# Optimization experiments

Hardware: AMD Instinct MI355X
Metric: run time of the kernel (lower is better)

The kernel has to match this reference:

```python
import jax, jax.numpy as jnp
import numpy as np

EMB = 1024
HEADS = 16
HEAD_DIM = EMB // HEADS


def setup_inputs() -> dict:
    key = jax.random.key(0)
    ks = jax.random.split(key, 12)
    B, S = 4, 2048
    s = 1.0 / np.sqrt(EMB)
    inp = {
        "query": jax.random.normal(ks[0], (B, S, EMB), jnp.float32),
        "key": jax.random.normal(ks[1], (B, S, EMB), jnp.float32),
        "value": jax.random.normal(ks[2], (B, S, EMB), jnp.float32),
        "mask": jax.random.randint(ks[3], (B, 1, 1, S), 0, 2) > 0,
        "Wq": jax.random.normal(ks[4], (EMB, EMB), jnp.float32) * s,
        "bq": jax.random.normal(ks[5], (EMB,), jnp.float32) * s,
        "Wk": jax.random.normal(ks[6], (EMB, EMB), jnp.float32) * s,
        "bk": jax.random.normal(ks[7], (EMB,), jnp.float32) * s,
        "Wv": jax.random.normal(ks[8], (EMB, EMB), jnp.float32) * s,
        "bv": jax.random.normal(ks[9], (EMB,), jnp.float32) * s,
        "Wo": jax.random.normal(ks[10], (EMB, EMB), jnp.float32) * s,
        "bo": jax.random.normal(ks[11], (EMB,), jnp.float32) * s,
    }
    return inp


def _split(x):
    # (B, S, E) -> (B, H, S, D)
    B, S, _ = x.shape
    return x.reshape(B, S, HEADS, HEAD_DIM).transpose(0, 2, 1, 3)


def reference(query, key, value, mask, Wq, bq, Wk, bk, Wv, bv, Wo, bo):
    q = _split(query @ Wq + bq)
    k = _split(key @ Wk + bk)
    v = _split(value @ Wv + bv)
    scale = 1.0 / np.sqrt(HEAD_DIM).astype(np.float32)
    # (B, H, S, S) score matrix, explicitly materialized as in the original
    scores = jnp.einsum("bhqd,bhkd->bhqk", q, k) * scale
    scores = jnp.where(mask, scores, -jnp.inf)
    probs = jax.nn.softmax(scores, axis=-1)
    attn = jnp.einsum("bhqk,bhkd->bhqd", probs, v)
    B, _, S, _ = attn.shape
    out = attn.transpose(0, 2, 1, 3).reshape(B, S, EMB)
    return out @ Wo + bo
```

## Files before the change

kernel.cpp:

```cpp
#include <hip/hip_runtime.h>
#include <hip/hip_bf16.h>
#include <stdint.h>

#define EMB 1024
#define HEADS 16
#define HDIM 64
#define BATCH 4
#define SEQ 2048
#define MTOT (BATCH * SEQ)

typedef unsigned short u16;
typedef __attribute__((ext_vector_type(8))) short bf16x8;
typedef __attribute__((ext_vector_type(4))) float f32x4;

__device__ inline u16 f2bf(float f) {
    uint32_t u = __builtin_bit_cast(uint32_t, f);
    u += 0x7fffu + ((u >> 16) & 1u);
    return (u16)(u >> 16);
}

__device__ inline uint32_t pk2bf(float a, float b) {
    uint32_t ua = __builtin_bit_cast(uint32_t, a) + 0x8000u;
    uint32_t ub = __builtin_bit_cast(uint32_t, b) + 0x8000u;
    return (ua >> 16) | (ub & 0xffff0000u);
}

__device__ inline f32x4 mfma16(bf16x8 a, bf16x8 b, f32x4 c) {
    return __builtin_amdgcn_mfma_f32_16x16x32_bf16(a, b, c, 0, 0, 0);
}

#define GLDS16(gp, lp)                                                        \
    __builtin_amdgcn_global_load_lds(                                         \
        (const __attribute__((address_space(1))) void*)(gp),                  \
        (__attribute__((address_space(3))) void*)(lp), 16, 0, 0)

__global__ void mask_compact(const int* __restrict__ mask,
                             int* __restrict__ cnt, int* __restrict__ idx,
                             float* __restrict__ Msg) {
    __shared__ int ps[256];
    const int b = blockIdx.x, tid = threadIdx.x;
    const int* mp = mask + (size_t)b * SEQ;
    int m[8], s = 0;
#pragma unroll
    for (int e = 0; e < 8; ++e) {
        m[e] = mp[tid * 8 + e] ? 1 : 0;
        s += m[e];
    }
    ps[tid] = s;
    __syncthreads();
    for (int off = 1; off < 256; off <<= 1) {
        int v = (tid >= off) ? ps[tid - off] : 0;
        __syncthreads();
        if (tid >= off) ps[tid] += v;
        __syncthreads();
    }
    const int total = ps[255];
    int r = ps[tid] - s;
#pragma unroll
    for (int e = 0; e < 8; ++e)
        if (m[e]) idx[b * SEQ + r++] = tid * 8 + e;
    if (tid == 0) cnt[b] = total;
    for (int j = tid; j < SEQ; j += 256)
        Msg[b * SEQ + j] = (j < total) ? 0.0f : -30000.0f;
}

__global__ void gather_cast(const float* __restrict__ src,
                            const int* __restrict__ idx,
                            const int* __restrict__ cnt,
                            u16* __restrict__ dst) {
    const int row = blockIdx.x;
    const int b = row >> 11, j = row & (SEQ - 1);
    const int cn = cnt[b];
    const int cp = (cn + 127) & ~127;
    if (j >= cp) return;
    const int c4 = threadIdx.x;
    float4 v = {0.f, 0.f, 0.f, 0.f};
    if (j < cn) {
        const int srow = idx[b * SEQ + j];
        v = ((const float4*)(src + (size_t)(b * SEQ + srow) * EMB))[c4];
    }
    ushort4 o;
    o.x = f2bf(v.x); o.y = f2bf(v.y); o.z = f2bf(v.z); o.w = f2bf(v.w);
    ((ushort4*)(dst + (size_t)row * EMB))[c4] = o;
}

__global__ void cast_f32_bf16(const float* __restrict__ src,
                              u16* __restrict__ dst, int n4) {
    int i = blockIdx.x * blockDim.x + threadIdx.x;
    if (i >= n4) return;
    float4 v = ((const float4*)src)[i];
    ushort4 o;
    o.x = f2bf(v.x); o.y = f2bf(v.y); o.z = f2bf(v.z); o.w = f2bf(v.w);
    ((ushort4*)dst)[i] = o;
}

__global__ void transpose_cast(const float* __restrict__ W,
                               u16* __restrict__ Wt) {
    __shared__ u16 T[64][65];
    const int kb = blockIdx.y * 64, nb = blockIdx.x * 64;
    const int tr = threadIdx.x >> 4;
    const int tc = (threadIdx.x & 15) * 4;
#pragma unroll
    for (int j = 0; j < 4; ++j) {
        int r = tr + j * 16;
        float4 v = *(const float4*)&W[(size_t)(kb + r) * EMB + nb + tc];
        T[tc + 0][r] = f2bf(v.x);
        T[tc + 1][r] = f2bf(v.y);
        T[tc + 2][r] = f2bf(v.z);
        T[tc + 3][r] = f2bf(v.w);
    }
    __syncthreads();
#pragma unroll
    for (int j = 0; j < 4; ++j) {
        int rr = tr + j * 16;
        ushort4 o;
        o.x = T[rr][tc]; o.y = T[rr][tc + 1];
        o.z = T[rr][tc + 2]; o.w = T[rr][tc + 3];
        *(ushort4*)&Wt[(size_t)(nb + rr) * EMB + kb + tc] = o;
    }
}

__global__ void transpose_v(const u16* __restrict__ Vp, u16* __restrict__ Vt,
                            const int* __restrict__ cnt) {
    __shared__ u16 T[64][65];
    const int h = blockIdx.x;
    const int b = blockIdx.y >> 5;
    const int s0 = (blockIdx.y & 31) * 64;
    const int cp = (cnt[b] + 127) & ~127;
    if (s0 >= cp) return;
    const int tr = threadIdx.x >> 3;
    const int tc = (threadIdx.x & 7) * 8;
#pragma unroll
    for (int j = 0; j < 2; ++j) {
        int sr = tr + j * 32;
        uint4 v = *(const uint4*)&Vp[(size_t)(b * SEQ + s0 + sr) * EMB +
                                     h * 64 + tc];
        const u16* p = (const u16*)&v;
#pragma unroll
        for (int e = 0; e < 8; ++e) T[tc + e][sr] = p[e];
    }
    __syncthreads();
#pragma unroll
    for (int j = 0; j < 2; ++j) {
        int d = tr + j * 32;
        u16 tmp[8];
#pragma unroll
        for (int e = 0; e < 8; ++e) tmp[e] = T[d][tc + e];
        const int base32 = s0 + (tc & 32);
        const int p0 = ((tc & 8) << 1) + ((tc & 16) >> 2);
        const size_t rowoff =
            ((size_t)(b * HEADS + h) * HDIM + d) * SEQ;
        *(uint2*)&Vt[rowoff + base32 + p0] = *(const uint2*)&tmp[0];
        *(uint2*)&Vt[rowoff + base32 + p0 + 8] = *(const uint2*)&tmp[4];
    }
}

template <bool OUT_BF16>
__global__ __launch_bounds__(256, 2) void gemm_bt(
    const u16* __restrict__ A, const u16* __restrict__ Bt,
    const float* __restrict__ bias, void* __restrict__ C,
    int M, int N, int K, const int* __restrict__ cnt) {
    __shared__ __align__(16) u16 As[128 * 32];
    __shared__ __align__(16) u16 Bs[128 * 32];
    const int m0 = blockIdx.y * 128, n0 = blockIdx.x * 128;
    if (cnt) {
        const int bb = m0 >> 11;
        const int cp = (cnt[bb] + 127) & ~127;
        if ((m0 & (SEQ - 1)) >= cp) return;
    }
    const int tid = threadIdx.x;
    const int w = tid >> 6, l = tid & 63;
    const int quad = l >> 4, l16 = l & 15;
    const int wm = (w >> 1) * 64, wn = (w & 1) * 64;

    f32x4 acc[4][4];
#pragma unroll
    for (int i = 0; i < 4; ++i)
#pragma unroll
        for (int j = 0; j < 4; ++j) acc[i][j] = (f32x4){0.f, 0.f, 0.f, 0.f};

    for (int k0 = 0; k0 < K; k0 += 32) {
        __syncthreads();
#pragma unroll
        for (int i = 0; i < 2; ++i) {
            int c = (w * 2 + i) * 64 + l;
            int r = c >> 2;
            int sc = (c & 3) ^ ((r >> 1) & 3);
            GLDS16(A + (size_t)(m0 + r) * K + k0 + sc * 8, &As[c * 8]);
            GLDS16(Bt + (size_t)(n0 + r) * K + k0 + sc * 8, &Bs[c * 8]);
        }
        __syncthreads();
        bf16x8 af[4], bfr[4];
#pragma unroll
        for (int mt = 0; mt < 4; ++mt) {
            int ra = wm + mt * 16 + l16;
            af[mt] = *(const bf16x8*)&As[ra * 32 +
                                         ((quad ^ ((ra >> 1) & 3)) * 8)];
        }
#pragma unroll
        for (int nt = 0; nt < 4; ++nt) {
            int rb = wn + nt * 16 + l16;
            bfr[nt] = *(const bf16x8*)&Bs[rb * 32 +
                                          ((quad ^ ((rb >> 1) & 3)) * 8)];
        }
#pragma unroll
        for (int mt = 0; mt < 4; ++mt)
#pragma unroll
            for (int nt = 0; nt < 4; ++nt)
                acc[mt][nt] = mfma16(af[mt], bfr[nt], acc[mt][nt]);
    }

#pragma unroll
    for (int mt = 0; mt < 4; ++mt) {
#pragma unroll
        for (int nt = 0; nt < 4; ++nt) {
            int col = n0 + wn + nt * 16 + l16;
            float bv = bias[col];
#pragma unroll
            for (int r = 0; r < 4; ++r) {
                int row = m0 + wm + mt * 16 + quad * 4 + r;
                float v = acc[mt][nt][r] + bv;
                if (OUT_BF16)
                    ((u16*)C)[(size_t)row * N + col] = f2bf(v);
                else
                    ((float*)C)[(size_t)row * N + col] = v;
            }
        }
    }
}

__global__ __launch_bounds__(256, 2) void attn_kernel(
    const u16* __restrict__ Qp, const u16* __restrict__ Kp,
    const u16* __restrict__ Vt, const float* __restrict__ Msg,
    const int* __restrict__ cnt, u16* __restrict__ attnb) {
    __shared__ __align__(16) u16 Ks[2][128 * 64];
    __shared__ __align__(16) u16 Vts[2][64 * 128];
    __shared__ __align__(16) float Ms[SEQ];

    const int tid = threadIdx.x;
    const int w = tid >> 6, l = tid & 63;
    const int quad = l >> 4, l16 = l & 15;

    const int nqb = SEQ / 128;
    const int qb = blockIdx.x % nqb;
    const int bh = blockIdx.x / nqb;
    const int b = bh / HEADS, h = bh % HEADS;
    const int q0 = qb * 128;
    const size_t head_off = (size_t)b * SEQ * EMB + (size_t)h * HDIM;
    const size_t vt_off = (size_t)bh * HDIM * SEQ;

    const int ntile = ((cnt[b] + 127) & ~127) >> 7;

    auto stageKV = [&](int buf, int t) {
#pragma unroll
        for (int i = 0; i < 4; ++i) {
            int c = (w * 4 + i) * 64 + l;
            int r = c >> 3;
            int sc = (c & 7) ^ (r & 7);
            GLDS16(Kp + head_off + (size_t)(t * 128 + r) * EMB + sc * 8,
                   &Ks[buf][c * 8]);
        }
#pragma unroll
        for (int i = 0; i < 4; ++i) {
            int c = (w * 4 + i) * 64 + l;
            int r = c >> 4;
            int sc = (c & 15) ^ (r & 15);
            GLDS16(Vt + vt_off + (size_t)r * SEQ + t * 128 + sc * 8,
                   &Vts[buf][c * 8]);
        }
    };

    bf16x8 bq[2][2];
#pragma unroll
    for (int g = 0; g < 2; ++g) {
        const u16* qrow =
            Qp + head_off + (size_t)(q0 + w * 32 + g * 16 + l16) * EMB;
        bq[g][0] = *(const bf16x8*)(qrow + quad * 8);
        bq[g][1] = *(const bf16x8*)(qrow + 32 + quad * 8);
    }

    {
        const float4* mg = (const float4*)(Msg + (size_t)b * SEQ);
        const int nf4 = ntile * 32;
        for (int j = tid; j < nf4; j += 256) ((float4*)Ms)[j] = mg[j];
    }
    stageKV(0, 0);
    __syncthreads();

    f32x4 OA[4], OB[4];
#pragma unroll
    for (int i = 0; i < 4; ++i) {
        OA[i] = (f32x4){0.f, 0.f, 0.f, 0.f};
        OB[i] = (f32x4){0.f, 0.f, 0.f, 0.f};
    }
    float lA = 0.f, lB = 0.f;
    const float c2 = 0.125f * 1.44269504f;

    for (int t = 0; t < ntile; ++t) {
        const int cur = t & 1;
        if (t + 1 < ntile) stageKV(cur ^ 1, t + 1);
        const u16* ksb = Ks[cur];
        const u16* vsb = Vts[cur];

        uint32_t pk[2][8][2];
        f32x4 ssum0 = (f32x4){0.f, 0.f, 0.f, 0.f};
        f32x4 ssum1 = (f32x4){0.f, 0.f, 0.f, 0.f};
#pragma unroll
        for (int nt = 0; nt < 8; ++nt) {
            int rk = nt * 16 + l16;
            bf16x8 ka0 =
                *(const bf16x8*)&ksb[rk * 64 + ((quad ^ (rk & 7)) * 8)];
            bf16x8 ka1 =
                *(const bf16x8*)&ksb[rk * 64 + (((quad + 4) ^ (rk & 7)) * 8)];
            f32x4 msb = *(const f32x4*)&Ms[t * 128 + nt * 16 + quad * 4];
#pragma unroll
            for (int g = 0; g < 2; ++g) {
                f32x4 s = (f32x4){0.f, 0.f, 0.f, 0.f};
                s = mfma16(ka0, bq[g][0], s);
                s = mfma16(ka1, bq[g][1], s);
                f32x4 p;
#pragma unroll
                for (int r = 0; r < 4; ++r)
                    p[r] = __builtin_amdgcn_exp2f(fmaf(s[r], c2, msb[r]));
                if (g == 0) ssum0 += p; else ssum1 += p;
                pk[g][nt][0] = pk2bf(p[0], p[1]);
                pk[g][nt][1] = pk2bf(p[2], p[3]);
            }
        }
        {
            float ts = (ssum0[0] + ssum0[1]) + (ssum0[2] + ssum0[3]);
            ts += __shfl_xor(ts, 16);
            ts += __shfl_xor(ts, 32);
            lA += ts;
            float tu = (ssum1[0] + ssum1[1]) + (ssum1[2] + ssum1[3]);
            tu += __shfl_xor(tu, 16);
            tu += __shfl_xor(tu, 32);
            lB += tu;
        }

#pragma unroll
        for (int i = 0; i < 4; ++i) {
            union { bf16x8 v; uint32_t u[4]; } bpA, bpB;
            bpA.u[0] = pk[0][2 * i][0];
            bpA.u[1] = pk[0][2 * i][1];
            bpA.u[2] = pk[0][2 * i + 1][0];
            bpA.u[3] = pk[0][2 * i + 1][1];
            bpB.u[0] = pk[1][2 * i][0];
            bpB.u[1] = pk[1][2 * i][1];
            bpB.u[2] = pk[1][2 * i + 1][0];
            bpB.u[3] = pk[1][2 * i + 1][1];
#pragma unroll
            for (int dt = 0; dt < 4; ++dt) {
                int vd = dt * 16 + l16;
                bf16x8 ap = *(const bf16x8*)&vsb[vd * 128 +
                                                 (((4 * i + quad) ^ (vd & 15)) *
                                                  8)];
                OA[dt] = mfma16(ap, bpA.v, OA[dt]);
                OB[dt] = mfma16(ap, bpB.v, OB[dt]);
            }
        }

        __syncthreads();
    }

#pragma unroll
    for (int g = 0; g < 2; ++g) {
        float inv = 1.0f / (g == 0 ? lA : lB);
        const f32x4* O = (g == 0) ? OA : OB;
        const int orow = q0 + w * 32 + g * 16 + l16;
#pragma unroll
        for (int dt = 0; dt < 4; ++dt) {
            ushort4 o;
            o.x = f2bf(O[dt][0] * inv);
            o.y = f2bf(O[dt][1] * inv);
            o.z = f2bf(O[dt][2] * inv);
            o.w = f2bf(O[dt][3] * inv);
            *(uint2*)&attnb[head_off + (size_t)orow * EMB + dt * 16 +
                            quad * 4] = *(uint2*)&o;
        }
    }
}

extern "C" void kernel_launch(void* const* d_in, const int* in_sizes, int n_in,
                              void* d_out, int out_size, void* d_ws,
                              size_t ws_size, hipStream_t stream) {
    const float* query = (const float*)d_in[0];
    const float* key = (const float*)d_in[1];
    const float* value = (const float*)d_in[2];
    const int* mask = (const int*)d_in[3];
    const float* Wq = (const float*)d_in[4];
    const float* bq = (const float*)d_in[5];
    const float* Wk = (const float*)d_in[6];
    const float* bk = (const float*)d_in[7];
    const float* Wv = (const float*)d_in[8];
    const float* bv = (const float*)d_in[9];
    const float* Wo = (const float*)d_in[10];
    const float* bo = (const float*)d_in[11];

    char* ws = (char*)d_ws;
    const size_t MB = 1ull << 20;
    u16* xq = (u16*)(ws + 0 * MB);
    u16* xk = (u16*)(ws + 16 * MB);
    u16* xv = (u16*)(ws + 32 * MB);
    u16* Wqt = (u16*)(ws + 48 * MB);
    u16* Wkt = (u16*)(ws + 50 * MB);
    u16* Wvt = (u16*)(ws + 52 * MB);
    u16* Wot = (u16*)(ws + 54 * MB);
    u16* Qp = (u16*)(ws + 56 * MB);
    u16* Kp = (u16*)(ws + 72 * MB);
    u16* Vp = (u16*)(ws + 88 * MB);
    u16* attnb = (u16*)(ws + 104 * MB);
    u16* Vt = xq;

    int* cnt = (int*)d_out;
    int* idx = (int*)d_out + 64;
    float* Msg = (float*)d_out + 64 + MTOT;

    mask_compact<<<BATCH, 256, 0, stream>>>(mask, cnt, idx, Msg);

    const int n4 = MTOT * EMB / 4;
    cast_f32_bf16<<<(n4 + 255) / 256, 256, 0, stream>>>(query, xq, n4);
    gather_cast<<<MTOT, 256, 0, stream>>>(key, idx, cnt, xk);
    gather_cast<<<MTOT, 256, 0, stream>>>(value, idx, cnt, xv);

    dim3 tgrid(EMB / 64, EMB / 64);
    transpose_cast<<<tgrid, 256, 0, stream>>>(Wq, Wqt);
    transpose_cast<<<tgrid, 256, 0, stream>>>(Wk, Wkt);
    transpose_cast<<<tgrid, 256, 0, stream>>>(Wv, Wvt);
    transpose_cast<<<tgrid, 256, 0, stream>>>(Wo, Wot);

    dim3 ggrid(EMB / 128, MTOT / 128);
    gemm_bt<true><<<ggrid, 256, 0, stream>>>(xq, Wqt, bq, Qp, MTOT, EMB, EMB,
                                             nullptr);
    gemm_bt<true><<<ggrid, 256, 0, stream>>>(xk, Wkt, bk, Kp, MTOT, EMB, EMB,
                                             cnt);
    gemm_bt<true><<<ggrid, 256, 0, stream>>>(xv, Wvt, bv, Vp, MTOT, EMB, EMB,
                                             cnt);

    transpose_v<<<dim3(HEADS, MTOT / 64), 256, 0, stream>>>(Vp, Vt, cnt);

    attn_kernel<<<BATCH * HEADS * (SEQ / 128), 256, 0, stream>>>(Qp, Kp, Vt,
                                                                 Msg, cnt,
                                                                 attnb);

    gemm_bt<false><<<ggrid, 256, 0, stream>>>(attnb, Wot, bo, d_out, MTOT, EMB,
                                              EMB, nullptr);
}
```

Measured before the change: 345.5 us.

## Fold softmax scale into Q projection, compute row sums via MFMA, drop mask buffer

Folds the softmax scale and log2e factor into the Q projection epilogue, so the attention inner loop applies exp2 directly to the scores. The mask buffer and its LDS staging are removed; masking is applied only on the final tile through an index comparison against the compacted count. Row sums now come from an MFMA against a ones vector instead of VALU adds plus cross-lane shuffles. This trades some extra MFMA work for fewer VALU and LDS operations, at the cost of rounding Q after scaling in bf16.

```diff
diff --git a/kernel.cpp b/kernel.cpp
--- a/kernel.cpp
+++ b/kernel.cpp
@@ -35,8 +35,7 @@
         (__attribute__((address_space(3))) void*)(lp), 16, 0, 0)
 
 __global__ void mask_compact(const int* __restrict__ mask,
-                             int* __restrict__ cnt, int* __restrict__ idx,
-                             float* __restrict__ Msg) {
+                             int* __restrict__ cnt, int* __restrict__ idx) {
     __shared__ int ps[256];
     const int b = blockIdx.x, tid = threadIdx.x;
     const int* mp = mask + (size_t)b * SEQ;
@@ -60,8 +59,6 @@
     for (int e = 0; e < 8; ++e)
         if (m[e]) idx[b * SEQ + r++] = tid * 8 + e;
     if (tid == 0) cnt[b] = total;
-    for (int j = tid; j < SEQ; j += 256)
-        Msg[b * SEQ + j] = (j < total) ? 0.0f : -30000.0f;
 }
 
 __global__ void gather_cast(const float* __restrict__ src,
@@ -159,7 +156,7 @@
 __global__ __launch_bounds__(256, 2) void gemm_bt(
     const u16* __restrict__ A, const u16* __restrict__ Bt,
     const float* __restrict__ bias, void* __restrict__ C,
-    int M, int N, int K, const int* __restrict__ cnt) {
+    int M, int N, int K, float scale, const int* __restrict__ cnt) {
     __shared__ __align__(16) u16 As[128 * 32];
     __shared__ __align__(16) u16 Bs[128 * 32];
     const int m0 = blockIdx.y * 128, n0 = blockIdx.x * 128;
@@ -219,7 +216,7 @@
 #pragma unroll
             for (int r = 0; r < 4; ++r) {
                 int row = m0 + wm + mt * 16 + quad * 4 + r;
-                float v = acc[mt][nt][r] + bv;
+                float v = (acc[mt][nt][r] + bv) * scale;
                 if (OUT_BF16)
                     ((u16*)C)[(size_t)row * N + col] = f2bf(v);
                 else
@@ -231,11 +228,10 @@
 
 __global__ __launch_bounds__(256, 2) void attn_kernel(
     const u16* __restrict__ Qp, const u16* __restrict__ Kp,
-    const u16* __restrict__ Vt, const float* __restrict__ Msg,
-    const int* __restrict__ cnt, u16* __restrict__ attnb) {
+    const u16* __restrict__ Vt, const int* __restrict__ cnt,
+    u16* __restrict__ attnb) {
     __shared__ __align__(16) u16 Ks[2][128 * 64];
     __shared__ __align__(16) u16 Vts[2][64 * 128];
-    __shared__ __align__(16) float Ms[SEQ];
 
     const int tid = threadIdx.x;
     const int w = tid >> 6, l = tid & 63;
@@ -249,7 +245,8 @@
     const size_t head_off = (size_t)b * SEQ * EMB + (size_t)h * HDIM;
     const size_t vt_off = (size_t)bh * HDIM * SEQ;
 
-    const int ntile = ((cnt[b] + 127) & ~127) >> 7;
+    const int cn = cnt[b];
+    const int ntile = ((cn + 127) & ~127) >> 7;
 
     auto stageKV = [&](int buf, int t) {
 #pragma unroll
@@ -279,11 +276,10 @@
         bq[g][1] = *(const bf16x8*)(qrow + 32 + quad * 8);
     }
 
-    {
-        const float4* mg = (const float4*)(Msg + (size_t)b * SEQ);
-        const int nf4 = ntile * 32;
-        for (int j = tid; j < nf4; j += 256) ((float4*)Ms)[j] = mg[j];
-    }
+    bf16x8 ones;
+#pragma unroll
+    for (int e = 0; e < 8; ++e) ones[e] = (short)0x3f80;
+
     stageKV(0, 0);
     __syncthreads();
 
@@ -293,18 +289,16 @@
         OA[i] = (f32x4){0.f, 0.f, 0.f, 0.f};
         OB[i] = (f32x4){0.f, 0.f, 0.f, 0.f};
     }
-    float lA = 0.f, lB = 0.f;
-    const float c2 = 0.125f * 1.44269504f;
-
-    for (int t = 0; t < ntile; ++t) {
+    f32x4 LA = (f32x4){0.f, 0.f, 0.f, 0.f};
+    f32x4 LB = (f32x4){0.f, 0.f, 0.f, 0.f};
+
+    auto tilebody = [&](int t, bool last) {
         const int cur = t & 1;
-        if (t + 1 < ntile) stageKV(cur ^ 1, t + 1);
+        if (!last) stageKV(cur ^ 1, t + 1);
         const u16* ksb = Ks[cur];
         const u16* vsb = Vts[cur];
 
         uint32_t pk[2][8][2];
-        f32x4 ssum0 = (f32x4){0.f, 0.f, 0.f, 0.f};
-        f32x4 ssum1 = (f32x4){0.f, 0.f, 0.f, 0.f};
 #pragma unroll
         for (int nt = 0; nt < 8; ++nt) {
             int rk = nt * 16 + l16;
@@ -312,30 +306,26 @@
                 *(const bf16x8*)&ksb[rk * 64 + ((quad ^ (rk & 7)) * 8)];
             bf16x8 ka1 =
                 *(const bf16x8*)&ksb[rk * 64 + (((quad + 4) ^ (rk & 7)) * 8)];
-            f32x4 msb = *(const f32x4*)&Ms[t * 128 + nt * 16 + quad * 4];
 #pragma unroll
             for (int g = 0; g < 2; ++g) {
                 f32x4 s = (f32x4){0.f, 0.f, 0.f, 0.f};
                 s = mfma16(ka0, bq[g][0], s);
                 s = mfma16(ka1, bq[g][1], s);
                 f32x4 p;
-#pragma unroll
-                for (int r = 0; r < 4; ++r)
-                    p[r] = __builtin_amdgcn_exp2f(fmaf(s[r], c2, msb[r]));
-                if (g == 0) ssum0 += p; else ssum1 += p;
+                if (last) {
+                    const int kb = t * 128 + nt * 16 + quad * 4;
+#pragma unroll
+                    for (int r = 0; r < 4; ++r)
+                        p[r] = __builtin_amdgcn_exp2f(
+                            (kb + r < cn) ? s[r] : -30000.f);
+                } else {
+#pragma unroll
+                    for (int r = 0; r < 4; ++r)
+                        p[r] = __builtin_amdgcn_exp2f(s[r]);
+                }
                 pk[g][nt][0] = pk2bf(p[0], p[1]);
                 pk[g][nt][1] = pk2bf(p[2], p[3]);
             }
-        }
-        {
-            float ts = (ssum0[0] + ssum0[1]) + (ssum0[2] + ssum0[3]);
-            ts += __shfl_xor(ts, 16);
-            ts += __shfl_xor(ts, 32);
-            lA += ts;
-            float tu = (ssum1[0] + ssum1[1]) + (ssum1[2] + ssum1[3]);
-            tu += __shfl_xor(tu, 16);
-            tu += __shfl_xor(tu, 32);
-            lB += tu;
         }
 
 #pragma unroll
@@ -349,6 +339,8 @@
             bpB.u[1] = pk[1][2 * i][1];
             bpB.u[2] = pk[1][2 * i + 1][0];
             bpB.u[3] = pk[1][2 * i + 1][1];
+            LA = mfma16(ones, bpA.v, LA);
+            LB = mfma16(ones, bpB.v, LB);
 #pragma unroll
             for (int dt = 0; dt < 4; ++dt) {
                 int vd = dt * 16 + l16;
@@ -361,11 +353,14 @@
         }
 
         __syncthreads();
-    }
+    };
+
+    for (int t = 0; t < ntile - 1; ++t) tilebody(t, false);
+    tilebody(ntile - 1, true);
 
 #pragma unroll
     for (int g = 0; g < 2; ++g) {
-        float inv = 1.0f / (g == 0 ? lA : lB);
+        float inv = 1.0f / (g == 0 ? LA[0] : LB[0]);
         const f32x4* O = (g == 0) ? OA : OB;
         const int orow = q0 + w * 32 + g * 16 + l16;
 #pragma unroll
@@ -414,9 +409,8 @@
 
     int* cnt = (int*)d_out;
     int* idx = (int*)d_out + 64;
-    float* Msg = (float*)d_out + 64 + MTOT;
-
-    mask_compact<<<BATCH, 256, 0, stream>>>(mask, cnt, idx, Msg);
+
+    mask_compact<<<BATCH, 256, 0, stream>>>(mask, cnt, idx);
 
     const int n4 = MTOT * EMB / 4;
     cast_f32_bf16<<<(n4 + 255) / 256, 256, 0, stream>>>(query, xq, n4);
@@ -429,20 +423,20 @@
     transpose_cast<<<tgrid, 256, 0, stream>>>(Wv, Wvt);
     transpose_cast<<<tgrid, 256, 0, stream>>>(Wo, Wot);
 
+    const float c2 = 0.125f * 1.44269504f;
     dim3 ggrid(EMB / 128, MTOT / 128);
     gemm_bt<true><<<ggrid, 256, 0, stream>>>(xq, Wqt, bq, Qp, MTOT, EMB, EMB,
-                                             nullptr);
+                                             c2, nullptr);
     gemm_bt<true><<<ggrid, 256, 0, stream>>>(xk, Wkt, bk, Kp, MTOT, EMB, EMB,
-                                             cnt);
+                                             1.0f, cnt);
     gemm_bt<true><<<ggrid, 256, 0, stream>>>(xv, Wvt, bv, Vp, MTOT, EMB, EMB,
-                                             cnt);
+                                             1.0f, cnt);
 
     transpose_v<<<dim3(HEADS, MTOT / 64), 256, 0, stream>>>(Vp, Vt, cnt);
 
     attn_kernel<<<BATCH * HEADS * (SEQ / 128), 256, 0, stream>>>(Qp, Kp, Vt,
-                                                                 Msg, cnt,
-                                                                 attnb);
+                                                                 cnt, attnb);
 
     gemm_bt<false><<<ggrid, 256, 0, stream>>>(attnb, Wot, bo, d_out, MTOT, EMB,
-                                              EMB, nullptr);
-}
+                                              EMB, 1.0f, nullptr);
+}
```

Result: no change. 341.0 us (-1.3%).
